# Kernel tuning notes

Hardware: AMD Instinct MI355X
Metric: run time of the kernel (lower is better)

Reference implementation:

```python
import jax, jax.numpy as jnp
import numpy as np

B, C, N, M, H = 2, 512, 2048, 2048, 8
HD = C // H
SCALE = HD ** -0.5


def setup_inputs() -> dict:
    key = jax.random.key(0)
    ks = jax.random.split(key, 8)
    x = jax.random.normal(ks[0], (B, C, N), dtype=jnp.float32)
    y = jax.random.normal(ks[1], (B, C, M), dtype=jnp.float32)
    # linear weights stored as [in, out] so out = in @ W (equivalent to torch Linear)
    Wq = jax.random.normal(ks[2], (C, C), dtype=jnp.float32) * (C ** -0.5)
    Wkv = jax.random.normal(ks[3], (C, 2 * C), dtype=jnp.float32) * (C ** -0.5)
    # depthwise Conv1d, kernel_size=1, groups=C -> per-channel scale + bias
    lw = jax.random.normal(ks[4], (C,), dtype=jnp.float32)
    lb = jax.random.normal(ks[5], (C,), dtype=jnp.float32) * 0.01
    Wp = jax.random.normal(ks[6], (C, C), dtype=jnp.float32) * (C ** -0.5)
    bp = jax.random.normal(ks[7], (C,), dtype=jnp.float32) * 0.01
    return {"x": x, "y": y, "Wq": Wq, "Wkv": Wkv, "lw": lw, "lb": lb, "Wp": Wp, "bp": bp}


def reference(x, y, Wq, Wkv, lw, lb, Wp, bp):
    # x: [B,C,N], y: [B,C,M]
    q = (x.transpose(0, 2, 1) @ Wq).reshape(B, N, H, HD).transpose(0, 2, 1, 3)  # [B,H,N,HD]
    kv = (y.transpose(0, 2, 1) @ Wkv).reshape(B, M, H, HD, 2).transpose(0, 2, 1, 3, 4)
    k, v = kv[..., 0], kv[..., 1]  # [B,H,M,HD]
    attn = jax.nn.softmax(jnp.einsum('bhnd,bhmd->bhnm', q, k) * SCALE, axis=-1)
    # depthwise conv1d (ksize=1) on v laid out as [B,C,M]; channel c = h*HD + d
    lw2 = lw.reshape(H, HD)[None, :, None, :]
    lb2 = lb.reshape(H, HD)[None, :, None, :]
    v = v + v * lw2 + lb2
    out = jnp.einsum('bhnm,bhmd->bhnd', attn, v).transpose(0, 2, 1, 3).reshape(B, N, C)
    out = (out @ Wp + bp).transpose(0, 2, 1)  # [B,C,N]
    return out
```

## Files before the change

### kernel.cpp

```cpp
#include <hip/hip_runtime.h>

#define Bb 2
#define Cc 512
#define Nn 2048
#define Mm 2048
#define Hh 8
#define HD 64
#define QSCALE 0.18033688011112042f

typedef unsigned short u16;
typedef unsigned int u32;
typedef __bf16 bf16x8 __attribute__((ext_vector_type(8)));
typedef float f32x16 __attribute__((ext_vector_type(16)));

union V4 {
    uint4 u;
    bf16x8 b;
};

__device__ __forceinline__ u16 f2bfu(float f) {
    unsigned int b = __float_as_uint(f);
    unsigned int r = (b + 0x7fffu + ((b >> 16) & 1u)) >> 16;
    return (u16)r;
}
__device__ __forceinline__ float bfu2f(u16 u) {
    return __uint_as_float(((unsigned int)u) << 16);
}
__device__ __forceinline__ u32 pkbf(float lo, float hi_) {
    return __builtin_amdgcn_perm(__float_as_uint(hi_) + 0x8000u,
                                 __float_as_uint(lo) + 0x8000u, 0x07060302u);
}

__global__ __launch_bounds__(256) void transpose_all(
    const float* __restrict__ x, const float* __restrict__ y, const float* __restrict__ Wq,
    const float* __restrict__ Wkv, const float* __restrict__ Wp, u16* __restrict__ xT,
    u16* __restrict__ yT, u16* __restrict__ WqT, u16* __restrict__ WkvT,
    u16* __restrict__ WpT) {
    __shared__ float tile[32][33];
    const int z = blockIdx.z;
    const float* in;
    u16* out;
    int S, sx = blockIdx.x;
    size_t base = 0;
    const int R = 512;
    if (z < 4) {
        in = (z < 2) ? x : y;
        out = (z < 2) ? xT : yT;
        S = 2048;
        base = (size_t)(z & 1) * R * S;
    } else {
        if (sx < 16) {
            in = Wq; out = WqT; S = 512;
        } else if (sx < 48) {
            in = Wkv; out = WkvT; S = 1024; sx -= 16;
        } else {
            in = Wp; out = WpT; S = 512; sx -= 48;
        }
    }
    int r0 = blockIdx.y * 32, s0 = sx * 32;
    int tx = threadIdx.x, ty = threadIdx.y;
#pragma unroll
    for (int k = 0; k < 4; k++)
        tile[ty + 8 * k][tx] = in[base + (size_t)(r0 + ty + 8 * k) * S + s0 + tx];
    __syncthreads();
#pragma unroll
    for (int k = 0; k < 4; k++)
        out[base + (size_t)(s0 + ty + 8 * k) * R + r0 + tx] = f2bfu(tile[tx][ty + 8 * k]);
}

__global__ __launch_bounds__(256) void proj_qkv(const u16* __restrict__ xT,
                                                const u16* __restrict__ yT,
                                                const u16* __restrict__ WqT,
                                                const u16* __restrict__ WkvT,
                                                const float* __restrict__ lw,
                                                const float* __restrict__ lb,
                                                u16* __restrict__ qb, u16* __restrict__ kb,
                                                u16* __restrict__ vtb) {
    __shared__ alignas(16) u16 As[2][128 * 64];
    __shared__ alignas(16) u16 Bs[2][64 * 64];
    const int t = threadIdx.x;
    const int lane = t & 63, w = t >> 6;
    const int r = lane & 31, hi = lane >> 5;
    const bool isQ = (blockIdx.x < 8);
    const int c0 = (isQ ? blockIdx.x : blockIdx.x - 8) * 64;
    const int r0 = blockIdx.y * 128;
    const int wr = (w & 1) * 64, wc = (w >> 1) * 32;
    const u16* A = isQ ? xT : yT;
    const u16* Bt = isQ ? WqT : WkvT;

    const int sra = t >> 3, ska = t & 7;
    const int swa = ((ska ^ (sra & 7)) << 3);
    const u16* Ag = A + (size_t)(r0 + sra) * 512 + ska * 8;
    const u16* Bg = Bt + (size_t)(c0 + sra) * 512 + ska * 8;

    {
#pragma unroll
        for (int i = 0; i < 4; i++)
            *(uint4*)&As[0][(sra + 32 * i) * 64 + swa] = *(const uint4*)(Ag + (size_t)i * 32 * 512);
#pragma unroll
        for (int i = 0; i < 2; i++)
            *(uint4*)&Bs[0][(sra + 32 * i) * 64 + swa] = *(const uint4*)(Bg + (size_t)i * 32 * 512);
    }
    __syncthreads();

    f32x16 acc[2];
#pragma unroll
    for (int rs = 0; rs < 2; rs++)
#pragma unroll
        for (int e = 0; e < 16; e++) acc[rs][e] = 0.f;

    const int ra0 = wr + r, ra1 = wr + 32 + r, rb = wc + r;

    for (int kk = 0; kk < 8; kk++) {
        const int cur = kk & 1;
        uint4 pa[4], pb[2];
        const bool more = (kk < 7);
        if (more) {
            const size_t ko = (size_t)(kk + 1) * 64;
#pragma unroll
            for (int i = 0; i < 4; i++) pa[i] = *(const uint4*)(Ag + (size_t)i * 32 * 512 + ko);
#pragma unroll
            for (int i = 0; i < 2; i++) pb[i] = *(const uint4*)(Bg + (size_t)i * 32 * 512 + ko);
        }
        V4 af[2][4], bf[4];
#pragma unroll
        for (int ks = 0; ks < 4; ks++) {
            const int c = 2 * ks + hi;
            bf[ks].u = *(const uint4*)&Bs[cur][rb * 64 + ((c ^ (rb & 7)) << 3)];
            af[0][ks].u = *(const uint4*)&As[cur][ra0 * 64 + ((c ^ (ra0 & 7)) << 3)];
            af[1][ks].u = *(const uint4*)&As[cur][ra1 * 64 + ((c ^ (ra1 & 7)) << 3)];
        }
#pragma unroll
        for (int ks = 0; ks < 4; ks++) {
            acc[0] = __builtin_amdgcn_mfma_f32_32x32x16_bf16(af[0][ks].b, bf[ks].b, acc[0], 0, 0, 0);
            acc[1] = __builtin_amdgcn_mfma_f32_32x32x16_bf16(af[1][ks].b, bf[ks].b, acc[1], 0, 0, 0);
        }
        if (more) {
            const int nxt = cur ^ 1;
#pragma unroll
            for (int i = 0; i < 4; i++) *(uint4*)&As[nxt][(sra + 32 * i) * 64 + swa] = pa[i];
#pragma unroll
            for (int i = 0; i < 2; i++) *(uint4*)&Bs[nxt][(sra + 32 * i) * 64 + swa] = pb[i];
        }
        __syncthreads();
    }

    const int cg = c0 + wc + r;
    if (isQ) {
#pragma unroll
        for (int rs = 0; rs < 2; rs++)
#pragma unroll
            for (int e = 0; e < 16; e++) {
                int m = r0 + wr + rs * 32 + 4 * hi + (e & 3) + 8 * (e >> 2);
                qb[(size_t)m * 512 + cg] = f2bfu(acc[rs][e] * QSCALE);
            }
    } else {
        const int hd = cg >> 1, s = cg & 1, h = hd >> 6, d = hd & 63;
        const int bq = r0 >> 11;
        const int bh = bq * 8 + h;
        const int mb = (r0 & 2047) + wr + 4 * hi;
        if (s == 0) {
            u16* kbase = kb + ((size_t)bh * 2048) * 64 + d;
#pragma unroll
            for (int rs = 0; rs < 2; rs++)
#pragma unroll
                for (int e = 0; e < 16; e++) {
                    int m = mb + rs * 32 + (e & 3) + 8 * (e >> 2);
                    kbase[(size_t)m * 64] = f2bfu(acc[rs][e]);
                }
        } else {
            const float sw = 1.0f + lw[hd], sb = lb[hd];
            u16* vbase = vtb + ((size_t)bh * 64 + d) * 2048;
#pragma unroll
            for (int rs = 0; rs < 2; rs++)
#pragma unroll
                for (int eg = 0; eg < 4; eg++) {
                    int m = mb + rs * 32 + 8 * eg;
                    float v0 = acc[rs][4 * eg + 0] * sw + sb;
                    float v1 = acc[rs][4 * eg + 1] * sw + sb;
                    float v2 = acc[rs][4 * eg + 2] * sw + sb;
                    float v3 = acc[rs][4 * eg + 3] * sw + sb;
                    uint2 pk;
                    pk.x = pkbf(v0, v1);
                    pk.y = pkbf(v2, v3);
                    *(uint2*)(vbase + m) = pk;
                }
        }
    }
}

__global__ __launch_bounds__(256, 3) void flash_attn(const u16* __restrict__ q,
                                                     const u16* __restrict__ kk,
                                                     const u16* __restrict__ vt,
                                                     u16* __restrict__ po,
                                                     float* __restrict__ ls) {
    __shared__ alignas(16) u16 Ks[2][64 * 64];
    __shared__ alignas(16) u16 Vs[2][64 * 64];
    const int t = threadIdx.x;
    const int lane = t & 63, w = t >> 6;
    const int r = lane & 31, hi = lane >> 5;
    const int id = blockIdx.x;
    const int xcd = id & 7, sid = id >> 3;
    const int combo = xcd * 16 + (sid >> 3);
    const int nt = sid & 7;
    const int bh = combo >> 3, sp = combo & 7;
    const int b = bh >> 3, h = bh & 7;
    const int nw0 = nt * 256 + 64 * w + r;
    const int MT0 = sp * 4, MT1 = MT0 + 4;

    V4 qf[2][4];
    {
        const u16* qrow = q + ((size_t)(b * Nn + nw0)) * Cc + h * HD + hi * 8;
#pragma unroll
        for (int ks = 0; ks < 4; ks++) {
            qf[0][ks].u = *(const uint4*)(qrow + ks * 16);
            qf[1][ks].u = *(const uint4*)(qrow + 32 * Cc + ks * 16);
        }
    }

    const u16* kbase = kk + ((size_t)bh) * Mm * HD;
    const u16* vbase = vt + ((size_t)bh) * HD * Mm;

    const int cr0 = t >> 3, cc0 = t & 7;
    const int cr1 = cr0 + 32, cc1 = cc0;
    const int swa0 = cr0 * 64 + ((cc0 ^ (cr0 & 7)) << 3);
    const int swa1 = cr1 * 64 + ((cc1 ^ (cr1 & 7)) << 3);

    {
        int m00 = MT0 * 64;
        uint4 a0 = *(const uint4*)(kbase + (size_t)(m00 + cr0) * HD + cc0 * 8);
        uint4 a1 = *(const uint4*)(kbase + (size_t)(m00 + cr1) * HD + cc1 * 8);
        uint4 b0 = *(const uint4*)(vbase + (size_t)cr0 * Mm + m00 + cc0 * 8);
        uint4 b1 = *(const uint4*)(vbase + (size_t)cr1 * Mm + m00 + cc1 * 8);
        *(uint4*)&Ks[0][swa0] = a0;
        *(uint4*)&Ks[0][swa1] = a1;
        *(uint4*)&Vs[0][swa0] = b0;
        *(uint4*)&Vs[0][swa1] = b1;
    }
    __syncthreads();

    f32x16 oa[2][2];
#pragma unroll
    for (int v = 0; v < 2; v++)
#pragma unroll
        for (int nh = 0; nh < 2; nh++)
#pragma unroll
            for (int e = 0; e < 16; e++) oa[v][nh][e] = 0.f;
    float lsum0 = 0.f, lsum1 = 0.f;

    for (int mt = MT0; mt < MT1; mt++) {
        const int cur = mt & 1;
        uint4 nk0, nk1, nv0, nv1;
        const bool more = (mt + 1 < MT1);
        if (more) {
            int m0 = (mt + 1) * 64;
            nk0 = *(const uint4*)(kbase + (size_t)(m0 + cr0) * HD + cc0 * 8);
            nk1 = *(const uint4*)(kbase + (size_t)(m0 + cr1) * HD + cc1 * 8);
            nv0 = *(const uint4*)(vbase + (size_t)cr0 * Mm + m0 + cc0 * 8);
            nv1 = *(const uint4*)(vbase + (size_t)cr1 * Mm + m0 + cc1 * 8);
        }
#pragma unroll
        for (int s = 0; s < 2; s++) {
            f32x16 sa0, sa1;
#pragma unroll
            for (int e = 0; e < 16; e++) {
                sa0[e] = 0.f;
                sa1[e] = 0.f;
            }
#pragma unroll
            for (int ks = 0; ks < 4; ks++) {
                V4 af;
                af.u = *(const uint4*)&Ks[cur][(32 * s + r) * 64 +
                                               (((2 * ks + hi) ^ (r & 7)) << 3)];
                sa0 = __builtin_amdgcn_mfma_f32_32x32x16_bf16(af.b, qf[0][ks].b, sa0, 0, 0, 0);
                sa1 = __builtin_amdgcn_mfma_f32_32x32x16_bf16(af.b, qf[1][ks].b, sa1, 0, 0, 0);
            }
            u32 p[2][8];
#pragma unroll
            for (int qq = 0; qq < 8; qq++) {
                float e0 = __builtin_amdgcn_exp2f(sa0[2 * qq]);
                float e1 = __builtin_amdgcn_exp2f(sa0[2 * qq + 1]);
                lsum0 += e0 + e1;
                p[0][qq] = pkbf(e0, e1);
                float f0 = __builtin_amdgcn_exp2f(sa1[2 * qq]);
                float f1 = __builtin_amdgcn_exp2f(sa1[2 * qq + 1]);
                lsum1 += f0 + f1;
                p[1][qq] = pkbf(f0, f1);
            }
            u32 xr[2][4];
#pragma unroll
            for (int nh = 0; nh < 2; nh++) {
                xr[nh][0] = __shfl_xor(hi ? p[nh][0] : p[nh][2], 32);
                xr[nh][1] = __shfl_xor(hi ? p[nh][1] : p[nh][3], 32);
                xr[nh][2] = __shfl_xor(hi ? p[nh][4] : p[nh][6], 32);
                xr[nh][3] = __shfl_xor(hi ? p[nh][5] : p[nh][7], 32);
            }
#pragma unroll
            for (int kl = 0; kl < 2; kl++) {
                V4 pf[2];
#pragma unroll
                for (int nh = 0; nh < 2; nh++) {
                    if (kl == 0) {
                        pf[nh].u.x = hi ? xr[nh][0] : p[nh][0];
                        pf[nh].u.y = hi ? xr[nh][1] : p[nh][1];
                        pf[nh].u.z = hi ? p[nh][2] : xr[nh][0];
                        pf[nh].u.w = hi ? p[nh][3] : xr[nh][1];
                    } else {
                        pf[nh].u.x = hi ? xr[nh][2] : p[nh][4];
                        pf[nh].u.y = hi ? xr[nh][3] : p[nh][5];
                        pf[nh].u.z = hi ? p[nh][6] : xr[nh][2];
                        pf[nh].u.w = hi ? p[nh][7] : xr[nh][3];
                    }
                }
                const int c = 4 * s + 2 * kl + hi;
                V4 vf0, vf1;
                vf0.u = *(const uint4*)&Vs[cur][r * 64 + ((c ^ (r & 7)) << 3)];
                vf1.u = *(const uint4*)&Vs[cur][(32 + r) * 64 + ((c ^ (r & 7)) << 3)];
                oa[0][0] = __builtin_amdgcn_mfma_f32_32x32x16_bf16(vf0.b, pf[0].b, oa[0][0], 0, 0, 0);
                oa[0][1] = __builtin_amdgcn_mfma_f32_32x32x16_bf16(vf0.b, pf[1].b, oa[0][1], 0, 0, 0);
                oa[1][0] = __builtin_amdgcn_mfma_f32_32x32x16_bf16(vf1.b, pf[0].b, oa[1][0], 0, 0, 0);
                oa[1][1] = __builtin_amdgcn_mfma_f32_32x32x16_bf16(vf1.b, pf[1].b, oa[1][1], 0, 0, 0);
            }
        }
        if (more) {
            const int nxt = cur ^ 1;
            *(uint4*)&Ks[nxt][swa0] = nk0;
            *(uint4*)&Ks[nxt][swa1] = nk1;
            *(uint4*)&Vs[nxt][swa0] = nv0;
            *(uint4*)&Vs[nxt][swa1] = nv1;
        }
        __syncthreads();
    }

    lsum0 += __shfl_xor(lsum0, 32);
    lsum1 += __shfl_xor(lsum1, 32);
    u16* pob = po + (((size_t)sp * 16 + bh) * 64) * 2048 + nw0;
#pragma unroll
    for (int e = 0; e < 16; e++) {
        int d0 = (e & 3) + 8 * (e >> 2) + 4 * hi;
        pob[(size_t)d0 * 2048] = f2bfu(oa[0][0][e]);
        pob[(size_t)(d0 + 32) * 2048] = f2bfu(oa[1][0][e]);
        pob[(size_t)d0 * 2048 + 32] = f2bfu(oa[0][1][e]);
        pob[(size_t)(d0 + 32) * 2048 + 32] = f2bfu(oa[1][1][e]);
    }
    if (hi == 0) {
        ls[((size_t)sp * 16 + bh) * 2048 + nw0] = lsum0;
        ls[((size_t)sp * 16 + bh) * 2048 + nw0 + 32] = lsum1;
    }
}

__global__ __launch_bounds__(256) void combine_o(const u16* __restrict__ po,
                                                 const float* __restrict__ ls,
                                                 u16* __restrict__ o) {
    __shared__ u16 tile[64][72];
    const int t = threadIdx.x;
    const int n0 = blockIdx.x * 64, bh = blockIdx.y;
    const int n = n0 + (t & 63), dg = t >> 6;
    float linv;
    {
        float s = 0.f;
#pragma unroll
        for (int sp = 0; sp < 8; sp++) s += ls[((size_t)sp * 16 + bh) * 2048 + n];
        linv = 1.0f / s;
    }
#pragma unroll
    for (int i = 0; i < 16; i++) {
        int d = dg * 16 + i;
        float acc = 0.f;
#pragma unroll
        for (int sp = 0; sp < 8; sp++)
            acc += bfu2f(po[(((size_t)sp * 16 + bh) * 64 + d) * 2048 + n]);
        tile[t & 63][d] = f2bfu(acc * linv);
    }
    __syncthreads();
    const int nr = t >> 2, dq = (t & 3) * 16;
    const int b = bh >> 3, h = bh & 7;
    u16* orow = o + ((size_t)(b * Nn + n0 + nr)) * Cc + h * 64 + dq;
    *(uint4*)(orow + 0) = *(const uint4*)&tile[nr][dq];
    *(uint4*)(orow + 8) = *(const uint4*)&tile[nr][dq + 8];
}

__global__ __launch_bounds__(256) void gemm_out(const u16* __restrict__ Wt,
                                                const u16* __restrict__ Ob,
                                                float* __restrict__ out,
                                                const float* __restrict__ bias) {
    __shared__ alignas(16) u16 Ws[2][64 * 64];
    __shared__ alignas(16) u16 Os[2][128 * 64];
    const int t = threadIdx.x;
    const int lane = t & 63, w = t >> 6;
    const int r = lane & 31, hi = lane >> 5;
    const int c0 = blockIdx.x * 64, n0 = blockIdx.y * 128;
    const int cb = (w & 1) * 32, nb = (w >> 1) * 32;

    const int sra = t >> 3, ska = t & 7;
    const int swa = ((ska ^ (sra & 7)) << 3);
    const u16* Wg = Wt + (size_t)(c0 + sra) * 512 + ska * 8;
    const u16* Og = Ob + (size_t)(n0 + sra) * 512 + ska * 8;

    {
#pragma unroll
        for (int i = 0; i < 2; i++)
            *(uint4*)&Ws[0][(sra + 32 * i) * 64 + swa] = *(const uint4*)(Wg + (size_t)i * 32 * 512);
#pragma unroll
        for (int i = 0; i < 4; i++)
            *(uint4*)&Os[0][(sra + 32 * i) * 64 + swa] = *(const uint4*)(Og + (size_t)i * 32 * 512);
    }
    __syncthreads();

    f32x16 acc[2];
#pragma unroll
    for (int ns = 0; ns < 2; ns++)
#pragma unroll
        for (int e = 0; e < 16; e++) acc[ns][e] = 0.f;

    const int rw = cb + r, ro0 = nb + r, ro1 = nb + 64 + r;

    for (int kk = 0; kk < 8; kk++) {
        const int cur = kk & 1;
        uint4 pw[2], po_[4];
        const bool more = (kk < 7);
        if (more) {
            const size_t ko = (size_t)(kk + 1) * 64;
#pragma unroll
            for (int i = 0; i < 2; i++) pw[i] = *(const uint4*)(Wg + (size_t)i * 32 * 512 + ko);
#pragma unroll
            for (int i = 0; i < 4; i++) po_[i] = *(const uint4*)(Og + (size_t)i * 32 * 512 + ko);
        }
        V4 wf[4], of[2][4];
#pragma unroll
        for (int ks = 0; ks < 4; ks++) {
            const int c = 2 * ks + hi;
            wf[ks].u = *(const uint4*)&Ws[cur][rw * 64 + ((c ^ (rw & 7)) << 3)];
            of[0][ks].u = *(const uint4*)&Os[cur][ro0 * 64 + ((c ^ (ro0 & 7)) << 3)];
            of[1][ks].u = *(const uint4*)&Os[cur][ro1 * 64 + ((c ^ (ro1 & 7)) << 3)];
        }
#pragma unroll
        for (int ks = 0; ks < 4; ks++) {
            acc[0] = __builtin_amdgcn_mfma_f32_32x32x16_bf16(wf[ks].b, of[0][ks].b, acc[0], 0, 0, 0);
            acc[1] = __builtin_amdgcn_mfma_f32_32x32x16_bf16(wf[ks].b, of[1][ks].b, acc[1], 0, 0, 0);
        }
        if (more) {
            const int nxt = cur ^ 1;
#pragma unroll
            for (int i = 0; i < 2; i++) *(uint4*)&Ws[nxt][(sra + 32 * i) * 64 + swa] = pw[i];
#pragma unroll
            for (int i = 0; i < 4; i++) *(uint4*)&Os[nxt][(sra + 32 * i) * 64 + swa] = po_[i];
        }
        __syncthreads();
    }

#pragma unroll
    for (int e = 0; e < 16; e++) {
        const int c_r = c0 + cb + 4 * hi + (e & 3) + 8 * (e >> 2);
        const float bv = bias[c_r];
#pragma unroll
        for (int ns = 0; ns < 2; ns++) {
            const int rg = n0 + nb + ns * 64 + r;
            const int b = rg >> 11, n = rg & 2047;
            out[((size_t)b * 512 + c_r) * 2048 + n] = acc[ns][e] + bv;
        }
    }
}

static const size_t OFF_XT = 0;
static const size_t OFF_YT = 4194304;
static const size_t OFF_WQT = 8388608;
static const size_t OFF_WKVT = 8912896;
static const size_t OFF_WPT = 9961472;
static const size_t OFF_Q = 10485760;
static const size_t OFF_K = 23068672;
static const size_t OFF_VT = 27262976;
static const size_t OFF_O = 31457280;
static const size_t OFF_PO = 35651584;
static const size_t OFF_LS = 69206016;

extern "C" void kernel_launch(void* const* d_in, const int* in_sizes, int n_in,
                              void* d_out, int out_size, void* d_ws, size_t ws_size,
                              hipStream_t stream) {
    const float* x = (const float*)d_in[0];
    const float* y = (const float*)d_in[1];
    const float* Wq = (const float*)d_in[2];
    const float* Wkv = (const float*)d_in[3];
    const float* lw = (const float*)d_in[4];
    const float* lb = (const float*)d_in[5];
    const float* Wp = (const float*)d_in[6];
    const float* bp = (const float*)d_in[7];

    char* ws = (char*)d_ws;
    u16* xT = (u16*)(ws + OFF_XT);
    u16* yT = (u16*)(ws + OFF_YT);
    u16* WqT = (u16*)(ws + OFF_WQT);
    u16* WkvT = (u16*)(ws + OFF_WKVT);
    u16* WpT = (u16*)(ws + OFF_WPT);
    u16* qb = (u16*)(ws + OFF_Q);
    u16* kb = (u16*)(ws + OFF_K);
    u16* vtb = (u16*)(ws + OFF_VT);
    u16* ob = (u16*)(ws + OFF_O);
    u16* po = (u16*)(ws + OFF_PO);
    float* lsw = (float*)(ws + OFF_LS);

    dim3 tb(32, 8, 1);
    transpose_all<<<dim3(64, 16, 5), tb, 0, stream>>>(x, y, Wq, Wkv, Wp, xT, yT, WqT, WkvT,
                                                      WpT);
    proj_qkv<<<dim3(24, 32), 256, 0, stream>>>(xT, yT, WqT, WkvT, lw, lb, qb, kb, vtb);
    flash_attn<<<dim3(1024), 256, 0, stream>>>(qb, kb, vtb, po, lsw);
    combine_o<<<dim3(Nn / 64, Bb * Hh), 256, 0, stream>>>(po, lsw, ob);
    gemm_out<<<dim3(8, 32), 256, 0, stream>>>(WpT, ob, (float*)d_out, bp);
}
```

Baseline: 155.1 us.

## Halve split-K partitions and store attention partials row-major via LDS staging

The key dimension is now split into 4 partitions of 8 tiles each instead of 8 partitions of 4, which halves the partial-output traffic and the grid size. Each wave stages its output accumulator through swizzled shared memory, so partials are written as coalesced 16-byte rows laid out [n][d] instead of strided 2-byte stores. The combine kernel now reads these rows with vector loads and no shared-memory transpose. The trade-offs are fewer blocks (512) with a lower occupancy hint, less parallelism, and longer per-block loops.

Result: faster. 134.5 us (-13.3%).

```diff
diff --git a/kernel.cpp b/kernel.cpp
--- a/kernel.cpp
+++ b/kernel.cpp
@@ -189,24 +189,23 @@
     }
 }
 
-__global__ __launch_bounds__(256, 3) void flash_attn(const u16* __restrict__ q,
+__global__ __launch_bounds__(256, 2) void flash_attn(const u16* __restrict__ q,
                                                      const u16* __restrict__ kk,
                                                      const u16* __restrict__ vt,
                                                      u16* __restrict__ po,
                                                      float* __restrict__ ls) {
-    __shared__ alignas(16) u16 Ks[2][64 * 64];
-    __shared__ alignas(16) u16 Vs[2][64 * 64];
+    __shared__ alignas(16) u16 SM[16384];
     const int t = threadIdx.x;
     const int lane = t & 63, w = t >> 6;
     const int r = lane & 31, hi = lane >> 5;
     const int id = blockIdx.x;
     const int xcd = id & 7, sid = id >> 3;
-    const int combo = xcd * 16 + (sid >> 3);
+    const int combo = xcd * 8 + (sid >> 3);
     const int nt = sid & 7;
-    const int bh = combo >> 3, sp = combo & 7;
+    const int bh = combo >> 2, sp = combo & 3;
     const int b = bh >> 3, h = bh & 7;
     const int nw0 = nt * 256 + 64 * w + r;
-    const int MT0 = sp * 4, MT1 = MT0 + 4;
+    const int MT0 = sp * 8, MT1 = MT0 + 8;
 
     V4 qf[2][4];
     {
@@ -232,10 +231,10 @@
         uint4 a1 = *(const uint4*)(kbase + (size_t)(m00 + cr1) * HD + cc1 * 8);
         uint4 b0 = *(const uint4*)(vbase + (size_t)cr0 * Mm + m00 + cc0 * 8);
         uint4 b1 = *(const uint4*)(vbase + (size_t)cr1 * Mm + m00 + cc1 * 8);
-        *(uint4*)&Ks[0][swa0] = a0;
-        *(uint4*)&Ks[0][swa1] = a1;
-        *(uint4*)&Vs[0][swa0] = b0;
-        *(uint4*)&Vs[0][swa1] = b1;
+        *(uint4*)&SM[swa0] = a0;
+        *(uint4*)&SM[swa1] = a1;
+        *(uint4*)&SM[8192 + swa0] = b0;
+        *(uint4*)&SM[8192 + swa1] = b1;
     }
     __syncthreads();
 
@@ -249,7 +248,8 @@
     float lsum0 = 0.f, lsum1 = 0.f;
 
     for (int mt = MT0; mt < MT1; mt++) {
-        const int cur = mt & 1;
+        const u16* Ksc = &SM[(mt & 1) * 4096];
+        const u16* Vsc = &SM[8192 + (mt & 1) * 4096];
         uint4 nk0, nk1, nv0, nv1;
         const bool more = (mt + 1 < MT1);
         if (more) {
@@ -270,8 +270,8 @@
 #pragma unroll
             for (int ks = 0; ks < 4; ks++) {
                 V4 af;
-                af.u = *(const uint4*)&Ks[cur][(32 * s + r) * 64 +
-                                               (((2 * ks + hi) ^ (r & 7)) << 3)];
+                af.u = *(const uint4*)&Ksc[(32 * s + r) * 64 +
+                                           (((2 * ks + hi) ^ (r & 7)) << 3)];
                 sa0 = __builtin_amdgcn_mfma_f32_32x32x16_bf16(af.b, qf[0][ks].b, sa0, 0, 0, 0);
                 sa1 = __builtin_amdgcn_mfma_f32_32x32x16_bf16(af.b, qf[1][ks].b, sa1, 0, 0, 0);
             }
@@ -314,8 +314,8 @@
                 }
                 const int c = 4 * s + 2 * kl + hi;
                 V4 vf0, vf1;
-                vf0.u = *(const uint4*)&Vs[cur][r * 64 + ((c ^ (r & 7)) << 3)];
-                vf1.u = *(const uint4*)&Vs[cur][(32 + r) * 64 + ((c ^ (r & 7)) << 3)];
+                vf0.u = *(const uint4*)&Vsc[r * 64 + ((c ^ (r & 7)) << 3)];
+                vf1.u = *(const uint4*)&Vsc[(32 + r) * 64 + ((c ^ (r & 7)) << 3)];
                 oa[0][0] = __builtin_amdgcn_mfma_f32_32x32x16_bf16(vf0.b, pf[0].b, oa[0][0], 0, 0, 0);
                 oa[0][1] = __builtin_amdgcn_mfma_f32_32x32x16_bf16(vf0.b, pf[1].b, oa[0][1], 0, 0, 0);
                 oa[1][0] = __builtin_amdgcn_mfma_f32_32x32x16_bf16(vf1.b, pf[0].b, oa[1][0], 0, 0, 0);
@@ -323,25 +323,41 @@
             }
         }
         if (more) {
-            const int nxt = cur ^ 1;
-            *(uint4*)&Ks[nxt][swa0] = nk0;
-            *(uint4*)&Ks[nxt][swa1] = nk1;
-            *(uint4*)&Vs[nxt][swa0] = nv0;
-            *(uint4*)&Vs[nxt][swa1] = nv1;
+            const int nxt = (mt & 1) ^ 1;
+            *(uint4*)&SM[nxt * 4096 + swa0] = nk0;
+            *(uint4*)&SM[nxt * 4096 + swa1] = nk1;
+            *(uint4*)&SM[8192 + nxt * 4096 + swa0] = nv0;
+            *(uint4*)&SM[8192 + nxt * 4096 + swa1] = nv1;
         }
         __syncthreads();
     }
 
     lsum0 += __shfl_xor(lsum0, 32);
     lsum1 += __shfl_xor(lsum1, 32);
-    u16* pob = po + (((size_t)sp * 16 + bh) * 64) * 2048 + nw0;
-#pragma unroll
-    for (int e = 0; e < 16; e++) {
-        int d0 = (e & 3) + 8 * (e >> 2) + 4 * hi;
-        pob[(size_t)d0 * 2048] = f2bfu(oa[0][0][e]);
-        pob[(size_t)(d0 + 32) * 2048] = f2bfu(oa[1][0][e]);
-        pob[(size_t)d0 * 2048 + 32] = f2bfu(oa[0][1][e]);
-        pob[(size_t)(d0 + 32) * 2048 + 32] = f2bfu(oa[1][1][e]);
+
+    u16* stg = &SM[w * 4096];
+#pragma unroll
+    for (int v = 0; v < 2; v++)
+#pragma unroll
+        for (int nh = 0; nh < 2; nh++)
+#pragma unroll
+            for (int g = 0; g < 4; g++) {
+                uint2 pk;
+                pk.x = pkbf(oa[v][nh][4 * g + 0], oa[v][nh][4 * g + 1]);
+                pk.y = pkbf(oa[v][nh][4 * g + 2], oa[v][nh][4 * g + 3]);
+                const int row = r + 32 * nh;
+                const int c8 = g + 4 * v;
+                *(uint2*)&stg[row * 64 + ((c8 ^ (row & 7)) << 3) + 4 * hi] = pk;
+            }
+    __syncthreads();
+    const int W0 = nt * 256 + 64 * w;
+    u16* pob = po + (((size_t)sp * 16 + bh) * 2048 + W0) * 64;
+#pragma unroll
+    for (int pp = 0; pp < 8; pp++) {
+        const int nl = pp * 8 + (lane >> 3);
+        const int cc = lane & 7;
+        uint4 vv = *(const uint4*)&stg[nl * 64 + ((cc ^ (nl & 7)) << 3)];
+        *(uint4*)&pob[(size_t)nl * 64 + cc * 8] = vv;
     }
     if (hi == 0) {
         ls[((size_t)sp * 16 + bh) * 2048 + nw0] = lsum0;
@@ -352,32 +368,42 @@
 __global__ __launch_bounds__(256) void combine_o(const u16* __restrict__ po,
                                                  const float* __restrict__ ls,
                                                  u16* __restrict__ o) {
-    __shared__ u16 tile[64][72];
     const int t = threadIdx.x;
     const int n0 = blockIdx.x * 64, bh = blockIdx.y;
-    const int n = n0 + (t & 63), dg = t >> 6;
-    float linv;
-    {
-        float s = 0.f;
-#pragma unroll
-        for (int sp = 0; sp < 8; sp++) s += ls[((size_t)sp * 16 + bh) * 2048 + n];
-        linv = 1.0f / s;
-    }
-#pragma unroll
-    for (int i = 0; i < 16; i++) {
-        int d = dg * 16 + i;
-        float acc = 0.f;
-#pragma unroll
-        for (int sp = 0; sp < 8; sp++)
-            acc += bfu2f(po[(((size_t)sp * 16 + bh) * 64 + d) * 2048 + n]);
-        tile[t & 63][d] = f2bfu(acc * linv);
-    }
-    __syncthreads();
-    const int nr = t >> 2, dq = (t & 3) * 16;
-    const int b = bh >> 3, h = bh & 7;
-    u16* orow = o + ((size_t)(b * Nn + n0 + nr)) * Cc + h * 64 + dq;
-    *(uint4*)(orow + 0) = *(const uint4*)&tile[nr][dq];
-    *(uint4*)(orow + 8) = *(const uint4*)&tile[nr][dq + 8];
+    const int nn = t >> 2, dq = (t & 3) * 16;
+    const int n = n0 + nn;
+    float s = 0.f;
+#pragma unroll
+    for (int sp = 0; sp < 4; sp++) s += ls[((size_t)sp * 16 + bh) * 2048 + n];
+    const float linv = 1.0f / s;
+    float acc[16];
+#pragma unroll
+    for (int i = 0; i < 16; i++) acc[i] = 0.f;
+#pragma unroll
+    for (int sp = 0; sp < 4; sp++) {
+        const u16* pr = po + (((size_t)sp * 16 + bh) * 2048 + n) * 64 + dq;
+        uint4 a = *(const uint4*)pr;
+        uint4 b = *(const uint4*)(pr + 8);
+        const u16* pa = (const u16*)&a;
+        const u16* pb = (const u16*)&b;
+#pragma unroll
+        for (int i = 0; i < 8; i++) {
+            acc[i] += bfu2f(pa[i]);
+            acc[8 + i] += bfu2f(pb[i]);
+        }
+    }
+    const int b_ = bh >> 3, h = bh & 7;
+    u16* orow = o + ((size_t)(b_ * Nn + n)) * Cc + h * 64 + dq;
+    uint4 o0, o1;
+    u32* q0 = (u32*)&o0;
+    u32* q1 = (u32*)&o1;
+#pragma unroll
+    for (int i = 0; i < 4; i++) {
+        q0[i] = pkbf(acc[2 * i] * linv, acc[2 * i + 1] * linv);
+        q1[i] = pkbf(acc[8 + 2 * i] * linv, acc[8 + 2 * i + 1] * linv);
+    }
+    *(uint4*)orow = o0;
+    *(uint4*)(orow + 8) = o1;
 }
 
 __global__ __launch_bounds__(256) void gemm_out(const u16* __restrict__ Wt,
@@ -503,7 +529,7 @@
     transpose_all<<<dim3(64, 16, 5), tb, 0, stream>>>(x, y, Wq, Wkv, Wp, xT, yT, WqT, WkvT,
                                                       WpT);
     proj_qkv<<<dim3(24, 32), 256, 0, stream>>>(xT, yT, WqT, WkvT, lw, lb, qb, kb, vtb);
-    flash_attn<<<dim3(1024), 256, 0, stream>>>(qb, kb, vtb, po, lsw);
-    combine_o<<<dim3(Nn / 64, Bb * Hh), 256, 0, stream>>>(po, lsw, ob);
+    flash_attn<<<dim3(512), 256, 0, stream>>>(qb, kb, vtb, po, lsw);
+    combine_o<<<dim3(32, 16), 256, 0, stream>>>(po, lsw, ob);
     gemm_out<<<dim3(8, 32), 256, 0, stream>>>(WpT, ob, (float*)d_out, bp);
 }
```
